# Kernel tuning notes

Measured on AMD Instinct MI355X. Metric: run time of the kernel, lower is better.

Reference implementation:

```python
import jax, jax.numpy as jnp
import numpy as np

B, T, D, K = 16, 2048, 256, 1024


def setup_inputs() -> dict:
    key = jax.random.key(0)
    k1, k2 = jax.random.split(key)
    z_e_x = jax.random.normal(k1, (B, T, D), dtype=jnp.float32)
    # torch init is uniform(-1/K, 1/K); use normal scaled similarly for a realistic trained codebook
    embedding = jax.random.normal(k2, (K, D), dtype=jnp.float32)
    return {"z_e_x": z_e_x, "embedding": embedding}


def _vq_indices(inputs_flat, codebook):
    codebook_sqr = jnp.sum(codebook * codebook, axis=1)            # [K]
    inputs_sqr = jnp.sum(inputs_flat * inputs_flat, axis=1, keepdims=True)  # [N,1]
    distances = inputs_sqr + codebook_sqr[None, :] - 2.0 * (inputs_flat @ codebook.T)  # [N,K]
    return jnp.argmin(distances, axis=1)                           # [N] int


def reference(z_e_x, embedding):
    Dd = embedding.shape[1]
    inputs_flat = z_e_x.reshape(-1, Dd)                 # [N, D]
    indices_flat = _vq_indices(inputs_flat, embedding)  # [N]
    codes = embedding[indices_flat].reshape(z_e_x.shape)  # gather lookup
    z_q_x = codes                                       # straight-through quantized output
    z_q_x_bar = codes                                   # eval mode: embedding unchanged, same gather
    indices = indices_flat.reshape(z_e_x.shape[:-1])
    return (z_q_x, z_q_x_bar, indices)
```

## Files before the change

kernel.cpp:

```cpp
#include <hip/hip_runtime.h>
#include <float.h>

constexpr int kD = 256;
constexpr int kK = 1024;
constexpr int kN = 16 * 2048;

using bf16x8 = __attribute__((ext_vector_type(8))) short;
using f32x16 = __attribute__((ext_vector_type(16))) float;
using u16x8  = __attribute__((ext_vector_type(8))) unsigned short;

__device__ __forceinline__ unsigned short f2bf(float x) {
    union { float f; unsigned u; } a; a.f = x;
    const unsigned u = a.u;
    return (unsigned short)((u + 0x7fffu + ((u >> 16) & 1u)) >> 16);
}
__device__ __forceinline__ float bf2f(unsigned short b) {
    union { unsigned u; float f; } a; a.u = ((unsigned)b) << 16;
    return a.f;
}

#define GLOAD_LDS16(GP, LP) \
    __builtin_amdgcn_global_load_lds((const __attribute__((address_space(1))) unsigned int*)(GP), \
                                     (__attribute__((address_space(3))) unsigned int*)(LP), 16, 0, 0)

__global__ void vq_split_all_kernel(const float* __restrict__ X, const float* __restrict__ E,
                                    unsigned short* __restrict__ xh, unsigned short* __restrict__ xm,
                                    unsigned short* __restrict__ xl,
                                    unsigned short* __restrict__ eh, unsigned short* __restrict__ em,
                                    unsigned short* __restrict__ el,
                                    float* __restrict__ csqr) {
    __shared__ float part[64][4];
    const int b   = blockIdx.x;
    const bool isE = b >= 512;
    const int RB  = isE ? b - 512 : b;
    const float* src = isE ? E : X;
    unsigned short* oh = isE ? eh : xh;
    unsigned short* om = isE ? em : xm;
    unsigned short* ol = isE ? el : xl;
    const int t = threadIdx.x;
    #pragma unroll
    for (int it = 0; it < 8; ++it) {
        const int u   = it * 256 + t;
        const int l   = u & 63;
        const int f   = (u >> 6) & 1;
        const int t16 = u >> 7;
        const int row = RB * 64 + f * 32 + (l & 31);
        const int d0  = t16 * 16 + (l >> 5) * 8;
        const float4 v0 = *reinterpret_cast<const float4*>(src + (size_t)row * kD + d0);
        const float4 v1 = *reinterpret_cast<const float4*>(src + (size_t)row * kD + d0 + 4);
        const float x[8] = {v0.x, v0.y, v0.z, v0.w, v1.x, v1.y, v1.z, v1.w};
        u16x8 H, M, L;
        #pragma unroll
        for (int e = 0; e < 8; ++e) {
            const unsigned short h = f2bf(x[e]);
            const float r1 = x[e] - bf2f(h);
            const unsigned short m = f2bf(r1);
            const float r2 = r1 - bf2f(m);
            const unsigned short lo = f2bf(r2);
            H[e] = (short)h; M[e] = (short)m; L[e] = (short)lo;
        }
        const size_t o = (size_t)RB * 16384 + (size_t)u * 8;
        *reinterpret_cast<u16x8*>(oh + o) = H;
        *reinterpret_cast<u16x8*>(om + o) = M;
        *reinterpret_cast<u16x8*>(ol + o) = L;
    }
    if (isE) {
        const int r = t >> 2, q = t & 3;
        const float* rp = E + (size_t)(RB * 64 + r) * kD + q * 64;
        float s = 0.0f;
        #pragma unroll
        for (int i = 0; i < 16; ++i) {
            const float4 v = reinterpret_cast<const float4*>(rp)[i];
            s += v.x * v.x + v.y * v.y + v.z * v.z + v.w * v.w;
        }
        part[r][q] = s;
        __syncthreads();
        if (t < 64) csqr[RB * 64 + t] = part[t][0] + part[t][1] + part[t][2] + part[t][3];
    }
}

__global__ __launch_bounds__(256, 2) void vq_gemm_kernel(
    const unsigned short* __restrict__ xh, const unsigned short* __restrict__ xm,
    const unsigned short* __restrict__ xl,
    const unsigned short* __restrict__ eh, const unsigned short* __restrict__ em,
    const unsigned short* __restrict__ el,
    const float* __restrict__ csqr,
    unsigned long long* __restrict__ rowkey)
{
    __shared__ bf16x8 smem[2][2304];
    const int tid  = threadIdx.x;
    const int lane = tid & 63;
    const int wid  = tid >> 6;
    const int wr   = wid >> 1;
    const int wc   = wid & 1;

    const int w    = blockIdx.x;
    const int xcd  = w & 7;
    const int slot = w >> 3;
    const int rbp  = xcd * 16 + (slot >> 3);
    const int cbp  = slot & 7;

    const unsigned short* gbase[9];
    int ldsoff[9];
    #pragma unroll
    for (int k2 = 0; k2 < 9; ++k2) {
        const int s = wid * 9 + k2;
        const bool isB = s >= 24;
        const int q   = isB ? s - 24 : s;
        const int grp = q / 6;
        const int rem = q % 6;
        const int f   = rem / 3;
        const int lv  = rem % 3;
        const unsigned short* img = isB ? (lv == 0 ? eh : lv == 1 ? em : el)
                                        : (lv == 0 ? xh : lv == 1 ? xm : xl);
        const int RBx = isB ? (cbp * 2 + grp) : (rbp * 4 + grp);
        gbase[k2] = img + (size_t)RBx * 16384 + f * 512 + lane * 8;
        ldsoff[k2] = (isB ? 1536 + q * 64 : q * 64);
    }

    f32x16 acc[4][2];
    #pragma unroll
    for (int m = 0; m < 4; ++m) { acc[m][0] = (f32x16)0.0f; acc[m][1] = (f32x16)0.0f; }

    int au[4], bu[2];
    #pragma unroll
    for (int m = 0; m < 4; ++m) au[m] = ((wr * 2 + (m >> 1)) * 6 + (m & 1) * 3) * 64 + lane;
    #pragma unroll
    for (int n = 0; n < 2; ++n) bu[n] = 1536 + (wc * 6 + n * 3) * 64 + lane;

#define MFMA(a, b, cacc) __builtin_amdgcn_mfma_f32_32x32x16_bf16(a, b, cacc, 0, 0, 0)
    auto compute_chunk = [&](const bf16x8* sb) {
        bf16x8 A0[4], A1[4], A2[4];
        #pragma unroll
        for (int m = 0; m < 4; ++m) {
            A0[m] = sb[au[m]]; A1[m] = sb[au[m] + 64]; A2[m] = sb[au[m] + 128];
        }
        __builtin_amdgcn_s_setprio(1);
        #pragma unroll
        for (int n = 0; n < 2; ++n) {
            const bf16x8 bh = sb[bu[n]], bm = sb[bu[n] + 64], bl = sb[bu[n] + 128];
            #pragma unroll
            for (int m = 0; m < 4; ++m) {
                f32x16 a5 = acc[m][n];
                a5 = MFMA(A0[m], bh, a5);
                a5 = MFMA(A0[m], bm, a5);
                a5 = MFMA(A1[m], bh, a5);
                a5 = MFMA(A0[m], bl, a5);
                a5 = MFMA(A2[m], bh, a5);
                a5 = MFMA(A1[m], bm, a5);
                acc[m][n] = a5;
            }
        }
        __builtin_amdgcn_s_setprio(0);
    };
#undef MFMA
#define MFMA(a, b, cacc) __builtin_amdgcn_mfma_f32_32x32x16_bf16(a, b, cacc, 0, 0, 0)

    #pragma unroll
    for (int k2 = 0; k2 < 9; ++k2) GLOAD_LDS16(gbase[k2], &smem[0][ldsoff[k2]]);
    #pragma unroll
    for (int k2 = 0; k2 < 9; ++k2) GLOAD_LDS16(gbase[k2] + 1024, &smem[1][ldsoff[k2]]);

    #pragma unroll 1
    for (int c = 0; c < 15; ++c) {
        const int cur = c & 1;
        asm volatile("s_waitcnt vmcnt(9)" ::: "memory");
        __builtin_amdgcn_s_barrier();
        asm volatile("" ::: "memory");
        compute_chunk(smem[cur]);
        asm volatile("" ::: "memory");
        __builtin_amdgcn_s_barrier();
        asm volatile("" ::: "memory");
        if (c < 14) {
            #pragma unroll
            for (int k2 = 0; k2 < 9; ++k2)
                GLOAD_LDS16(gbase[k2] + (size_t)(c + 2) * 1024, &smem[cur][ldsoff[k2]]);
        }
    }
    asm volatile("s_waitcnt vmcnt(0)" ::: "memory");
    __builtin_amdgcn_s_barrier();
    asm volatile("" ::: "memory");
    compute_chunk(smem[1]);
#undef MFMA

    const int lane31 = lane & 31;
    const int colbase = cbp * 128 + wc * 64;
    const float cs0 = csqr[colbase + lane31];
    const float cs1 = csqr[colbase + 32 + lane31];
    const int rowbase = rbp * 256 + wr * 128 + 4 * (lane >> 5);

    #pragma unroll
    for (int m = 0; m < 4; ++m) {
        #pragma unroll
        for (int r = 0; r < 16; ++r) {
            float bv = fmaf(-2.0f, acc[m][0][r], cs0);
            int   bi = colbase + lane31;
            const float v1 = fmaf(-2.0f, acc[m][1][r], cs1);
            if (v1 < bv) { bv = v1; bi = colbase + 32 + lane31; }
            #pragma unroll
            for (int mk = 16; mk >= 1; mk >>= 1) {
                const float ov = __shfl_xor(bv, mk);
                const int   oi = __shfl_xor(bi, mk);
                if (ov < bv || (ov == bv && oi < bi)) { bv = ov; bi = oi; }
            }
            if (lane31 == 0) {
                const int row = rowbase + m * 32 + (r & 3) + 8 * (r >> 2);
                unsigned kb = __float_as_uint(bv);
                kb = (bv < 0.0f) ? ~kb : (kb | 0x80000000u);
                atomicMin(&rowkey[row], ((unsigned long long)kb << 32) | (unsigned)bi);
            }
        }
    }
}

__global__ void vq_gather_kernel(const float* __restrict__ E,
                                 const unsigned long long* __restrict__ rowkey,
                                 float* __restrict__ zq, float* __restrict__ zqb,
                                 float* __restrict__ idxf) {
    const int row = blockIdx.x * 4 + (threadIdx.x >> 6);
    const int lane = threadIdx.x & 63;
    const unsigned k = (unsigned)(rowkey[row] & 0xFFFFFFFFull);
    const float4 v = reinterpret_cast<const float4*>(E + (size_t)k * kD)[lane];
    reinterpret_cast<float4*>(zq + (size_t)row * kD)[lane] = v;
    reinterpret_cast<float4*>(zqb + (size_t)row * kD)[lane] = v;
    if (lane == 0) idxf[row] = (float)k;
}

extern "C" void kernel_launch(void* const* d_in, const int* in_sizes, int n_in,
                              void* d_out, int out_size, void* d_ws, size_t ws_size,
                              hipStream_t stream) {
    const float* X = (const float*)d_in[0];
    const float* E = (const float*)d_in[1];

    float* out  = (float*)d_out;
    float* zq   = out;
    float* zqb  = out + (size_t)kN * kD;
    float* idxf = out + 2 * (size_t)kN * kD;

    char* ob = (char*)d_out;
    unsigned short* XIh = (unsigned short*)ob;
    unsigned short* XIm = XIh + (size_t)kN * kD;
    unsigned short* XIl = XIm + (size_t)kN * kD;

    char* ws = (char*)d_ws;
    unsigned long long* rowkey = (unsigned long long*)ws;
    float* csqr = (float*)(ws + (size_t)kN * 8);
    unsigned short* EIh = (unsigned short*)(ws + (size_t)kN * 8 + 4096);
    unsigned short* EIm = EIh + (size_t)kK * kD;
    unsigned short* EIl = EIm + (size_t)kK * kD;

    hipMemsetAsync(rowkey, 0xFF, (size_t)kN * 8, stream);
    vq_split_all_kernel<<<kN / 64 + kK / 64, 256, 0, stream>>>(
        X, E, XIh, XIm, XIl, EIh, EIm, EIl, csqr);
    vq_gemm_kernel<<<(kN / 256) * (kK / 128), 256, 0, stream>>>(
        XIh, XIm, XIl, EIh, EIm, EIl, csqr, rowkey);
    vq_gather_kernel<<<kN / 4, 256, 0, stream>>>(E, rowkey, zq, zqb, idxf);
}
```

Before: 250.7 us.

## Enlarge GEMM tile to 256x256 with 8 waves and phased single-buffer staging

The GEMM block grows from 4 to 8 waves and now covers 256 codebook columns instead of 128, which halves the grid and doubles reuse of each loaded X tile. The K-loop is rebuilt as six MFMA passes per chunk. Each pass loads only the fragments it needs from LDS and issues part of the next chunk's global-to-LDS copy in between, with barriers around every pass. This aims to cut global traffic per output and spread the loads across the compute. In exchange it adds many more barriers per chunk and waits for all outstanding loads at the end of every chunk, which weakens the earlier two-deep prefetch.

```diff
diff --git a/kernel.cpp b/kernel.cpp
--- a/kernel.cpp
+++ b/kernel.cpp
@@ -79,7 +79,7 @@
     }
 }
 
-__global__ __launch_bounds__(256, 2) void vq_gemm_kernel(
+__global__ __launch_bounds__(512, 2) void vq_gemm_kernel(
     const unsigned short* __restrict__ xh, const unsigned short* __restrict__ xm,
     const unsigned short* __restrict__ xl,
     const unsigned short* __restrict__ eh, const unsigned short* __restrict__ em,
@@ -87,24 +87,24 @@
     const float* __restrict__ csqr,
     unsigned long long* __restrict__ rowkey)
 {
-    __shared__ bf16x8 smem[2][2304];
+    __shared__ bf16x8 smem[2][3072];
     const int tid  = threadIdx.x;
     const int lane = tid & 63;
     const int wid  = tid >> 6;
-    const int wr   = wid >> 1;
-    const int wc   = wid & 1;
+    const int wr   = wid >> 2;
+    const int wc   = wid & 3;
 
     const int w    = blockIdx.x;
     const int xcd  = w & 7;
     const int slot = w >> 3;
-    const int rbp  = xcd * 16 + (slot >> 3);
-    const int cbp  = slot & 7;
-
-    const unsigned short* gbase[9];
-    int ldsoff[9];
-    #pragma unroll
-    for (int k2 = 0; k2 < 9; ++k2) {
-        const int s = wid * 9 + k2;
+    const int rbp  = xcd * 16 + (slot >> 2);
+    const int cbp  = slot & 3;
+
+    const unsigned short* gbase[6];
+    int ldsoff[6];
+    #pragma unroll
+    for (int k2 = 0; k2 < 6; ++k2) {
+        const int s = wid * 6 + k2;
         const bool isB = s >= 24;
         const int q   = isB ? s - 24 : s;
         const int grp = q / 6;
@@ -113,9 +113,9 @@
         const int lv  = rem % 3;
         const unsigned short* img = isB ? (lv == 0 ? eh : lv == 1 ? em : el)
                                         : (lv == 0 ? xh : lv == 1 ? xm : xl);
-        const int RBx = isB ? (cbp * 2 + grp) : (rbp * 4 + grp);
+        const int RBx = isB ? (cbp * 4 + grp) : (rbp * 4 + grp);
         gbase[k2] = img + (size_t)RBx * 16384 + f * 512 + lane * 8;
-        ldsoff[k2] = (isB ? 1536 + q * 64 : q * 64);
+        ldsoff[k2] = (isB ? 1536 : 0) + q * 64;
     }
 
     f32x16 acc[4][2];
@@ -128,63 +128,82 @@
     #pragma unroll
     for (int n = 0; n < 2; ++n) bu[n] = 1536 + (wc * 6 + n * 3) * 64 + lane;
 
-#define MFMA(a, b, cacc) __builtin_amdgcn_mfma_f32_32x32x16_bf16(a, b, cacc, 0, 0, 0)
-    auto compute_chunk = [&](const bf16x8* sb) {
-        bf16x8 A0[4], A1[4], A2[4];
-        #pragma unroll
-        for (int m = 0; m < 4; ++m) {
-            A0[m] = sb[au[m]]; A1[m] = sb[au[m] + 64]; A2[m] = sb[au[m] + 128];
-        }
-        __builtin_amdgcn_s_setprio(1);
-        #pragma unroll
-        for (int n = 0; n < 2; ++n) {
-            const bf16x8 bh = sb[bu[n]], bm = sb[bu[n] + 64], bl = sb[bu[n] + 128];
-            #pragma unroll
-            for (int m = 0; m < 4; ++m) {
-                f32x16 a5 = acc[m][n];
-                a5 = MFMA(A0[m], bh, a5);
-                a5 = MFMA(A0[m], bm, a5);
-                a5 = MFMA(A1[m], bh, a5);
-                a5 = MFMA(A0[m], bl, a5);
-                a5 = MFMA(A2[m], bh, a5);
-                a5 = MFMA(A1[m], bm, a5);
-                acc[m][n] = a5;
-            }
-        }
-        __builtin_amdgcn_s_setprio(0);
-    };
-#undef MFMA
-#define MFMA(a, b, cacc) __builtin_amdgcn_mfma_f32_32x32x16_bf16(a, b, cacc, 0, 0, 0)
-
-    #pragma unroll
-    for (int k2 = 0; k2 < 9; ++k2) GLOAD_LDS16(gbase[k2], &smem[0][ldsoff[k2]]);
-    #pragma unroll
-    for (int k2 = 0; k2 < 9; ++k2) GLOAD_LDS16(gbase[k2] + 1024, &smem[1][ldsoff[k2]]);
+#define BARRIER() do { asm volatile("" ::: "memory"); __builtin_amdgcn_s_barrier(); \
+                       asm volatile("" ::: "memory"); } while (0)
+#define LGK0() asm volatile("s_waitcnt lgkmcnt(0)" ::: "memory")
+#define MMPASS(AX, BX) do { \
+    __builtin_amdgcn_s_setprio(1); \
+    _Pragma("unroll") \
+    for (int n_ = 0; n_ < 2; ++n_) { \
+        _Pragma("unroll") \
+        for (int m_ = 0; m_ < 4; ++m_) \
+            acc[m_][n_] = __builtin_amdgcn_mfma_f32_32x32x16_bf16(AX[m_], BX[n_], acc[m_][n_], 0, 0, 0); \
+    } \
+    __builtin_amdgcn_s_setprio(0); \
+} while (0)
+#define STAGE2(P) do { if (st) { \
+    GLOAD_LDS16(gbase[2 * (P)] + co, &nb[ldsoff[2 * (P)]]); \
+    GLOAD_LDS16(gbase[2 * (P) + 1] + co, &nb[ldsoff[2 * (P) + 1]]); } } while (0)
+
+    #pragma unroll
+    for (int k2 = 0; k2 < 6; ++k2) GLOAD_LDS16(gbase[k2], &smem[0][ldsoff[k2]]);
+    asm volatile("s_waitcnt vmcnt(0)" ::: "memory");
+    BARRIER();
 
     #pragma unroll 1
-    for (int c = 0; c < 15; ++c) {
-        const int cur = c & 1;
-        asm volatile("s_waitcnt vmcnt(9)" ::: "memory");
-        __builtin_amdgcn_s_barrier();
-        asm volatile("" ::: "memory");
-        compute_chunk(smem[cur]);
-        asm volatile("" ::: "memory");
-        __builtin_amdgcn_s_barrier();
-        asm volatile("" ::: "memory");
-        if (c < 14) {
-            #pragma unroll
-            for (int k2 = 0; k2 < 9; ++k2)
-                GLOAD_LDS16(gbase[k2] + (size_t)(c + 2) * 1024, &smem[cur][ldsoff[k2]]);
-        }
-    }
-    asm volatile("s_waitcnt vmcnt(0)" ::: "memory");
-    __builtin_amdgcn_s_barrier();
-    asm volatile("" ::: "memory");
-    compute_chunk(smem[1]);
-#undef MFMA
+    for (int c = 0; c < 16; ++c) {
+        const bf16x8* sb = smem[c & 1];
+        bf16x8* nb = smem[(c + 1) & 1];
+        const bool st = (c < 15);
+        const size_t co = (size_t)(c + 1) * 1024;
+        bf16x8 A0[4], A1[4], A2[4], B0[2], B1[2], B2[2];
+
+        #pragma unroll
+        for (int m = 0; m < 4; ++m) A0[m] = sb[au[m]];
+        #pragma unroll
+        for (int n = 0; n < 2; ++n) B0[n] = sb[bu[n]];
+        STAGE2(0);
+        BARRIER(); LGK0();
+        MMPASS(A0, B0);
+        BARRIER();
+
+        #pragma unroll
+        for (int n = 0; n < 2; ++n) B1[n] = sb[bu[n] + 64];
+        STAGE2(1);
+        BARRIER(); LGK0();
+        MMPASS(A0, B1);
+        BARRIER();
+
+        #pragma unroll
+        for (int m = 0; m < 4; ++m) A1[m] = sb[au[m] + 64];
+        STAGE2(2);
+        BARRIER(); LGK0();
+        MMPASS(A1, B0);
+        BARRIER();
+
+        #pragma unroll
+        for (int n = 0; n < 2; ++n) B2[n] = sb[bu[n] + 128];
+        BARRIER(); LGK0();
+        MMPASS(A0, B2);
+        BARRIER();
+
+        #pragma unroll
+        for (int m = 0; m < 4; ++m) A2[m] = sb[au[m] + 128];
+        BARRIER(); LGK0();
+        MMPASS(A2, B0);
+        BARRIER();
+
+        MMPASS(A1, B1);
+        asm volatile("s_waitcnt vmcnt(0)" ::: "memory");
+        BARRIER();
+    }
+#undef STAGE2
+#undef MMPASS
+#undef LGK0
+#undef BARRIER
 
     const int lane31 = lane & 31;
-    const int colbase = cbp * 128 + wc * 64;
+    const int colbase = cbp * 256 + wc * 64;
     const float cs0 = csqr[colbase + lane31];
     const float cs1 = csqr[colbase + 32 + lane31];
     const int rowbase = rbp * 256 + wr * 128 + 4 * (lane >> 5);
@@ -252,7 +271,7 @@
     hipMemsetAsync(rowkey, 0xFF, (size_t)kN * 8, stream);
     vq_split_all_kernel<<<kN / 64 + kK / 64, 256, 0, stream>>>(
         X, E, XIh, XIm, XIl, EIh, EIm, EIl, csqr);
-    vq_gemm_kernel<<<(kN / 256) * (kK / 128), 256, 0, stream>>>(
+    vq_gemm_kernel<<<(kN / 256) * (kK / 256), 512, 0, stream>>>(
         XIh, XIm, XIl, EIh, EIm, EIl, csqr, rowkey);
     vq_gather_kernel<<<kN / 4, 256, 0, stream>>>(E, rowkey, zq, zqb, idxf);
 }
```

Result: no change. 248.8 us (-0.8%).

## Replace LDS double-buffered pipeline with direct global-to-register fragment loads

Applied to the files above, without the earlier changes.

The GEMM kernel no longer stages the tiles in shared memory with global_load_lds, barriers and double buffering. Each wave now loads its own bf16 fragments directly from global memory into registers and software-prefetches the high part of the next chunk. The MFMA order is regrouped into six passes over all accumulators, which interleaves independent accumulators between dependent MFMAs. This removes the LDS traffic and block barriers, but each A/B fragment is now fetched separately by every wave that uses it, so global/L2 traffic goes up and register pressure rises.

```diff
diff --git a/kernel.cpp b/kernel.cpp
--- a/kernel.cpp
+++ b/kernel.cpp
@@ -18,10 +18,6 @@
     union { unsigned u; float f; } a; a.u = ((unsigned)b) << 16;
     return a.f;
 }
-
-#define GLOAD_LDS16(GP, LP) \
-    __builtin_amdgcn_global_load_lds((const __attribute__((address_space(1))) unsigned int*)(GP), \
-                                     (__attribute__((address_space(3))) unsigned int*)(LP), 16, 0, 0)
 
 __global__ void vq_split_all_kernel(const float* __restrict__ X, const float* __restrict__ E,
                                     unsigned short* __restrict__ xh, unsigned short* __restrict__ xm,
@@ -87,7 +83,6 @@
     const float* __restrict__ csqr,
     unsigned long long* __restrict__ rowkey)
 {
-    __shared__ bf16x8 smem[2][2304];
     const int tid  = threadIdx.x;
     const int lane = tid & 63;
     const int wid  = tid >> 6;
@@ -98,93 +93,98 @@
     const int xcd  = w & 7;
     const int slot = w >> 3;
     const int rbp  = xcd * 16 + (slot >> 3);
-    const int cbp  = slot & 7;
-
-    const unsigned short* gbase[9];
-    int ldsoff[9];
-    #pragma unroll
-    for (int k2 = 0; k2 < 9; ++k2) {
-        const int s = wid * 9 + k2;
-        const bool isB = s >= 24;
-        const int q   = isB ? s - 24 : s;
-        const int grp = q / 6;
-        const int rem = q % 6;
-        const int f   = rem / 3;
-        const int lv  = rem % 3;
-        const unsigned short* img = isB ? (lv == 0 ? eh : lv == 1 ? em : el)
-                                        : (lv == 0 ? xh : lv == 1 ? xm : xl);
-        const int RBx = isB ? (cbp * 2 + grp) : (rbp * 4 + grp);
-        gbase[k2] = img + (size_t)RBx * 16384 + f * 512 + lane * 8;
-        ldsoff[k2] = (isB ? 1536 + q * 64 : q * 64);
-    }
+    const int cb   = slot & 7;
+
+    const size_t laneoff = (size_t)lane * 8;
+    const size_t abase = (size_t)(rbp * 4 + wr * 2) * 16384 + laneoff;
+    const size_t bbase = (size_t)(cb * 2 + wc) * 16384 + laneoff;
+    const unsigned short* pah = xh + abase;
+    const unsigned short* pam = xm + abase;
+    const unsigned short* pal = xl + abase;
+    const unsigned short* pbh = eh + bbase;
+    const unsigned short* pbm = em + bbase;
+    const unsigned short* pbl = el + bbase;
+
+#define FOA(m, c) ((size_t)((m) >> 1) * 16384 + ((m) & 1) * 512 + (size_t)(c) * 1024)
+#define FOB(n, c) ((size_t)(n) * 512 + (size_t)(c) * 1024)
+#define LD8(p) (*reinterpret_cast<const bf16x8*>(p))
 
     f32x16 acc[4][2];
     #pragma unroll
     for (int m = 0; m < 4; ++m) { acc[m][0] = (f32x16)0.0f; acc[m][1] = (f32x16)0.0f; }
 
-    int au[4], bu[2];
-    #pragma unroll
-    for (int m = 0; m < 4; ++m) au[m] = ((wr * 2 + (m >> 1)) * 6 + (m & 1) * 3) * 64 + lane;
-    #pragma unroll
-    for (int n = 0; n < 2; ++n) bu[n] = 1536 + (wc * 6 + n * 3) * 64 + lane;
-
-#define MFMA(a, b, cacc) __builtin_amdgcn_mfma_f32_32x32x16_bf16(a, b, cacc, 0, 0, 0)
-    auto compute_chunk = [&](const bf16x8* sb) {
-        bf16x8 A0[4], A1[4], A2[4];
-        #pragma unroll
-        for (int m = 0; m < 4; ++m) {
-            A0[m] = sb[au[m]]; A1[m] = sb[au[m] + 64]; A2[m] = sb[au[m] + 128];
-        }
-        __builtin_amdgcn_s_setprio(1);
-        #pragma unroll
-        for (int n = 0; n < 2; ++n) {
-            const bf16x8 bh = sb[bu[n]], bm = sb[bu[n] + 64], bl = sb[bu[n] + 128];
-            #pragma unroll
-            for (int m = 0; m < 4; ++m) {
-                f32x16 a5 = acc[m][n];
-                a5 = MFMA(A0[m], bh, a5);
-                a5 = MFMA(A0[m], bm, a5);
-                a5 = MFMA(A1[m], bh, a5);
-                a5 = MFMA(A0[m], bl, a5);
-                a5 = MFMA(A2[m], bh, a5);
-                a5 = MFMA(A1[m], bm, a5);
-                acc[m][n] = a5;
+#define MFMA_(a, b, c_) __builtin_amdgcn_mfma_f32_32x32x16_bf16(a, b, c_, 0, 0, 0)
+    auto cluster = [&](const bf16x8* Ah, const bf16x8* Bh,
+                       const bf16x8* Am, const bf16x8* Bm,
+                       const bf16x8* Al, const bf16x8* Bl) {
+        #pragma unroll
+        for (int n = 0; n < 2; ++n)
+            #pragma unroll
+            for (int m = 0; m < 4; ++m) acc[m][n] = MFMA_(Ah[m], Bh[n], acc[m][n]);
+        #pragma unroll
+        for (int n = 0; n < 2; ++n)
+            #pragma unroll
+            for (int m = 0; m < 4; ++m) acc[m][n] = MFMA_(Am[m], Bh[n], acc[m][n]);
+        #pragma unroll
+        for (int n = 0; n < 2; ++n)
+            #pragma unroll
+            for (int m = 0; m < 4; ++m) acc[m][n] = MFMA_(Ah[m], Bm[n], acc[m][n]);
+        #pragma unroll
+        for (int n = 0; n < 2; ++n)
+            #pragma unroll
+            for (int m = 0; m < 4; ++m) acc[m][n] = MFMA_(Am[m], Bm[n], acc[m][n]);
+        #pragma unroll
+        for (int n = 0; n < 2; ++n)
+            #pragma unroll
+            for (int m = 0; m < 4; ++m) acc[m][n] = MFMA_(Ah[m], Bl[n], acc[m][n]);
+        #pragma unroll
+        for (int n = 0; n < 2; ++n)
+            #pragma unroll
+            for (int m = 0; m < 4; ++m) acc[m][n] = MFMA_(Al[m], Bh[n], acc[m][n]);
+    };
+
+    bf16x8 hA[4], hB[2], gA[4], gB[2];
+    #pragma unroll
+    for (int m = 0; m < 4; ++m) hA[m] = LD8(pah + FOA(m, 0));
+    #pragma unroll
+    for (int n = 0; n < 2; ++n) hB[n] = LD8(pbh + FOB(n, 0));
+
+    #pragma unroll 1
+    for (int c = 0; c < 16; c += 2) {
+        {
+            bf16x8 mA[4], mB[2], lA[4], lB[2];
+            #pragma unroll
+            for (int m = 0; m < 4; ++m) { mA[m] = LD8(pam + FOA(m, c)); lA[m] = LD8(pal + FOA(m, c)); }
+            #pragma unroll
+            for (int n = 0; n < 2; ++n) { mB[n] = LD8(pbm + FOB(n, c)); lB[n] = LD8(pbl + FOB(n, c)); }
+            #pragma unroll
+            for (int m = 0; m < 4; ++m) gA[m] = LD8(pah + FOA(m, c + 1));
+            #pragma unroll
+            for (int n = 0; n < 2; ++n) gB[n] = LD8(pbh + FOB(n, c + 1));
+            cluster(hA, hB, mA, mB, lA, lB);
+        }
+        {
+            bf16x8 mA[4], mB[2], lA[4], lB[2];
+            #pragma unroll
+            for (int m = 0; m < 4; ++m) { mA[m] = LD8(pam + FOA(m, c + 1)); lA[m] = LD8(pal + FOA(m, c + 1)); }
+            #pragma unroll
+            for (int n = 0; n < 2; ++n) { mB[n] = LD8(pbm + FOB(n, c + 1)); lB[n] = LD8(pbl + FOB(n, c + 1)); }
+            if (c + 2 < 16) {
+                #pragma unroll
+                for (int m = 0; m < 4; ++m) hA[m] = LD8(pah + FOA(m, c + 2));
+                #pragma unroll
+                for (int n = 0; n < 2; ++n) hB[n] = LD8(pbh + FOB(n, c + 2));
             }
-        }
-        __builtin_amdgcn_s_setprio(0);
-    };
-#undef MFMA
-#define MFMA(a, b, cacc) __builtin_amdgcn_mfma_f32_32x32x16_bf16(a, b, cacc, 0, 0, 0)
-
-    #pragma unroll
-    for (int k2 = 0; k2 < 9; ++k2) GLOAD_LDS16(gbase[k2], &smem[0][ldsoff[k2]]);
-    #pragma unroll
-    for (int k2 = 0; k2 < 9; ++k2) GLOAD_LDS16(gbase[k2] + 1024, &smem[1][ldsoff[k2]]);
-
-    #pragma unroll 1
-    for (int c = 0; c < 15; ++c) {
-        const int cur = c & 1;
-        asm volatile("s_waitcnt vmcnt(9)" ::: "memory");
-        __builtin_amdgcn_s_barrier();
-        asm volatile("" ::: "memory");
-        compute_chunk(smem[cur]);
-        asm volatile("" ::: "memory");
-        __builtin_amdgcn_s_barrier();
-        asm volatile("" ::: "memory");
-        if (c < 14) {
-            #pragma unroll
-            for (int k2 = 0; k2 < 9; ++k2)
-                GLOAD_LDS16(gbase[k2] + (size_t)(c + 2) * 1024, &smem[cur][ldsoff[k2]]);
-        }
-    }
-    asm volatile("s_waitcnt vmcnt(0)" ::: "memory");
-    __builtin_amdgcn_s_barrier();
-    asm volatile("" ::: "memory");
-    compute_chunk(smem[1]);
-#undef MFMA
+            cluster(gA, gB, mA, mB, lA, lB);
+        }
+    }
+#undef MFMA_
+#undef LD8
+#undef FOA
+#undef FOB
 
     const int lane31 = lane & 31;
-    const int colbase = cbp * 128 + wc * 64;
+    const int colbase = cb * 128 + wc * 64;
     const float cs0 = csqr[colbase + lane31];
     const float cs1 = csqr[colbase + 32 + lane31];
     const int rowbase = rbp * 256 + wr * 128 + 4 * (lane >> 5);
```

After: 258.7 us. 1.03x slower.
